# Performance work log

Hardware: AMD Instinct MI355X
Metric: run time of the kernel (lower is better)

## Reference

```python
import jax, jax.numpy as jnp
import numpy as np
from jax import lax

H = 64          # GRU hidden size
OUT_STEPS = 20  # output_seq_size


def _maxpool2(x):
    # x: [N, C, H, W] -> 2x2 max pool, stride 2, VALID
    return lax.reduce_window(x, -jnp.inf, lax.max, (1, 1, 2, 2), (1, 1, 2, 2), 'VALID')


def _conv(x, w, b):
    # NCHW / OIHW, VALID, stride 1
    y = lax.conv_general_dilated(x, w, (1, 1), 'VALID',
                                 dimension_numbers=('NCHW', 'OIHW', 'NCHW'))
    return y + b[None, :, None, None]


def _gru_step(h, x, wih, whh, bih, bhh):
    # PyTorch GRU gate order: r, z, n
    gi = x @ wih.T + bih            # [B, 3H]
    gh = h @ whh.T + bhh            # [B, 3H]
    i_r, i_z, i_n = jnp.split(gi, 3, axis=-1)
    h_r, h_z, h_n = jnp.split(gh, 3, axis=-1)
    r = jax.nn.sigmoid(i_r + h_r)
    z = jax.nn.sigmoid(i_z + h_z)
    n = jnp.tanh(i_n + r * h_n)
    return (1.0 - z) * n + z * h


def setup_inputs() -> dict:
    key = jax.random.key(0)
    ks = jax.random.split(key, 20)
    B, T = 1024, 31
    s = 0.1
    return {
        'bbox_seq': jax.random.normal(ks[0], (B, T, 4), jnp.float32),
        'head_seq': jax.random.uniform(ks[1], (B, T, 32, 32), jnp.float32),
        'conv1_w': jax.random.normal(ks[2], (4, 1, 3, 3), jnp.float32) * s,
        'conv1_b': jax.random.normal(ks[3], (4,), jnp.float32) * s,
        'conv2_w': jax.random.normal(ks[4], (10, 4, 3, 3), jnp.float32) * s,
        'conv2_b': jax.random.normal(ks[5], (10,), jnp.float32) * s,
        'fc_w': jax.random.normal(ks[6], (5, 360), jnp.float32) * s,
        'fc_b': jax.random.normal(ks[7], (5,), jnp.float32) * s,
        'enc_wih': jax.random.normal(ks[8], (3 * H, 9), jnp.float32) * s,
        'enc_whh': jax.random.normal(ks[9], (3 * H, H), jnp.float32) * s,
        'enc_bih': jax.random.normal(ks[10], (3 * H,), jnp.float32) * s,
        'enc_bhh': jax.random.normal(ks[11], (3 * H,), jnp.float32) * s,
        'dec_wih': jax.random.normal(ks[12], (3 * H, 4), jnp.float32) * s,
        'dec_whh': jax.random.normal(ks[13], (3 * H, H), jnp.float32) * s,
        'dec_bih': jax.random.normal(ks[14], (3 * H,), jnp.float32) * s,
        'dec_bhh': jax.random.normal(ks[15], (3 * H,), jnp.float32) * s,
        'lin_w': jax.random.normal(ks[16], (4, H), jnp.float32) * s,
        'lin_b': jax.random.normal(ks[17], (4,), jnp.float32) * s,
    }


def reference(bbox_seq, head_seq, conv1_w, conv1_b, conv2_w, conv2_b, fc_w, fc_b,
              enc_wih, enc_whh, enc_bih, enc_bhh,
              dec_wih, dec_whh, dec_bih, dec_bhh, lin_w, lin_b):
    B, T = bbox_seq.shape[0], bbox_seq.shape[1]
    L = T - 1  # encoder sequence length

    # offset: last bbox, broadcast over OUT_STEPS -> [B, OUT_STEPS, 4]
    offset = jnp.broadcast_to(bbox_seq[:, -1][:, None, :], (B, OUT_STEPS, 4))

    diffs = bbox_seq[:, 1:] - bbox_seq[:, :-1]  # [B, L, 4] (dropout p=0 -> identity)

    # --- ConvEncoder on all head crops at once ---
    imgs = head_seq[:, :-1].reshape(B * L, 1, 32, 32)
    x = jax.nn.relu(_conv(imgs, conv1_w, conv1_b))   # [BL, 4, 30, 30]
    x = _maxpool2(x)                                  # [BL, 4, 15, 15]
    x = jax.nn.relu(_conv(x, conv2_w, conv2_b))       # [BL, 10, 13, 13]
    x = _maxpool2(x)                                  # [BL, 10, 6, 6]
    emb = x.reshape(B * L, -1) @ fc_w.T + fc_b        # [BL, 5]
    emb = emb.reshape(B, L, -1)

    enc_in = jnp.concatenate([diffs, emb], axis=2)    # [B, L, 9]

    # --- GRU encoder (scan over time) ---
    def enc_step(h, x_t):
        h = _gru_step(h, x_t, enc_wih, enc_whh, enc_bih, enc_bhh)
        return h, None
    h0 = jnp.zeros((B, H), enc_in.dtype)
    hn, _ = lax.scan(enc_step, h0, jnp.swapaxes(enc_in, 0, 1))

    def dec_step(carry, _):
        h, prev_x = carry
        h = _gru_step(h, prev_x, dec_wih, dec_whh, dec_bih, dec_bhh)
        x_new = h @ lin_w.T + lin_b + prev_x
        return (h, x_new), x_new
    (_, _), outs = lax.scan(dec_step, (hn, diffs[:, -1]), None, length=OUT_STEPS)
    out = jnp.swapaxes(outs, 0, 1)                    # [B, OUT_STEPS, 4]

    return jnp.cumsum(out, axis=1) + offset
```

## Files before the change

kernel.cpp:

```cpp
#include <hip/hip_runtime.h>
#include <hip/hip_bf16.h>


#define B_    1024
#define L_    30
#define H_    64

typedef _Float16 half_t;
typedef __attribute__((ext_vector_type(8))) _Float16 half8;
typedef __attribute__((ext_vector_type(4))) float f32x4;

#define MFMA16(A, B, C) __builtin_amdgcn_mfma_f32_16x16x32_f16(A, B, C, 0, 0, 0)

__device__ __forceinline__ float sigmoid_f(float v) {
    return __builtin_amdgcn_rcpf(1.f + __expf(-v));
}
__device__ __forceinline__ float tanh_f(float v) {
    v = fminf(fmaxf(v, -15.f), 15.f);
    const float e = __expf(2.f * v);
    return (e - 1.f) * __builtin_amdgcn_rcpf(e + 1.f);
}
__device__ __forceinline__ void load4_lds(float* r, const float* p) {
    float2 a = *(const float2*)p;
    float2 b = *(const float2*)(p + 2);
    r[0] = a.x; r[1] = a.y; r[2] = b.x; r[3] = b.y;
}

__global__ __launch_bounds__(64) void conv_embed_kernel(
    const float* __restrict__ bbox,
    const float* __restrict__ head,
    const float* __restrict__ c1w, const float* __restrict__ c1b,
    const float* __restrict__ c2w, const float* __restrict__ c2b,
    const float* __restrict__ fcw, const float* __restrict__ fcb,
    float* __restrict__ enc_in)
{
    const int img = blockIdx.x;
    const int b = img / L_;
    const int l = img % L_;
    const int tid = threadIdx.x;

    __shared__ float s_img[32 * 32];
    __shared__ float s_p1[4 * 15 * 16];
    __shared__ float s_p2[360];
    __shared__ float s_red[60];

    {
        const float4* src = (const float4*)(head + ((size_t)b * 31 + (size_t)l) * 1024);
        float4* dst = (float4*)s_img;
        #pragma unroll
        for (int i = 0; i < 4; ++i) dst[tid + 64 * i] = src[tid + 64 * i];
    }
    __syncthreads();

    if (tid < 60) {
        const int c = tid / 15, px = tid % 15;
        const int x0 = 2 * px;
        float wg[9];
        #pragma unroll
        for (int k = 0; k < 9; ++k) wg[k] = c1w[c * 9 + k];
        const float bias = c1b[c];

        auto c1out = [&](const float* ra, const float* rb, const float* rc, const float* rd) -> float {
            float a00 = bias, a01 = bias, a10 = bias, a11 = bias;
            #pragma unroll
            for (int kx = 0; kx < 3; ++kx) {
                const float w0 = wg[kx], w1 = wg[3 + kx], w2 = wg[6 + kx];
                a00 = fmaf(w0, ra[kx],     fmaf(w1, rb[kx],     fmaf(w2, rc[kx],     a00)));
                a01 = fmaf(w0, ra[kx + 1], fmaf(w1, rb[kx + 1], fmaf(w2, rc[kx + 1], a01)));
                a10 = fmaf(w0, rb[kx],     fmaf(w1, rc[kx],     fmaf(w2, rd[kx],     a10)));
                a11 = fmaf(w0, rb[kx + 1], fmaf(w1, rc[kx + 1], fmaf(w2, rd[kx + 1], a11)));
            }
            a00 = fmaxf(a00, 0.f); a01 = fmaxf(a01, 0.f);
            a10 = fmaxf(a10, 0.f); a11 = fmaxf(a11, 0.f);
            return fmaxf(fmaxf(a00, a01), fmaxf(a10, a11));
        };

        float r[6][4];
        load4_lds(r[0], s_img + 0 * 32 + x0);
        load4_lds(r[1], s_img + 1 * 32 + x0);
        #pragma unroll
        for (int i = 0; i < 7; ++i) {
            const int s0 = (4 * i) % 6, s1 = (4 * i + 1) % 6, s2 = (4 * i + 2) % 6;
            const int s3 = (4 * i + 3) % 6, s4 = (4 * i + 4) % 6, s5 = (4 * i + 5) % 6;
            load4_lds(r[s2], s_img + (4 * i + 2) * 32 + x0);
            load4_lds(r[s3], s_img + (4 * i + 3) * 32 + x0);
            s_p1[c * 240 + (2 * i) * 16 + px] = c1out(r[s0], r[s1], r[s2], r[s3]);
            load4_lds(r[s4], s_img + (4 * i + 4) * 32 + x0);
            load4_lds(r[s5], s_img + (4 * i + 5) * 32 + x0);
            s_p1[c * 240 + (2 * i + 1) * 16 + px] = c1out(r[s2], r[s3], r[s4], r[s5]);
        }
        load4_lds(r[0], s_img + 30 * 32 + x0);
        load4_lds(r[1], s_img + 31 * 32 + x0);
        s_p1[c * 240 + 14 * 16 + px] = c1out(r[4], r[5], r[0], r[1]);
    }
    __syncthreads();

    if (tid < 60) {
        const int c = tid / 6, px = tid % 6;
        const int x0 = 2 * px;
        float wg2[4][9];
        #pragma unroll
        for (int ic = 0; ic < 4; ++ic)
            #pragma unroll
            for (int k = 0; k < 9; ++k) wg2[ic][k] = c2w[(c * 4 + ic) * 9 + k];
        const float bias2 = c2b[c];

        float P[6][4][4];
        auto c2out = [&](float (*pa)[4], float (*pb)[4], float (*pc)[4], float (*pd)[4]) -> float {
            float a00 = bias2, a01 = bias2, a10 = bias2, a11 = bias2;
            #pragma unroll
            for (int ic = 0; ic < 4; ++ic) {
                #pragma unroll
                for (int kx = 0; kx < 3; ++kx) {
                    const float w0 = wg2[ic][kx], w1 = wg2[ic][3 + kx], w2 = wg2[ic][6 + kx];
                    a00 = fmaf(w0, pa[ic][kx],     fmaf(w1, pb[ic][kx],     fmaf(w2, pc[ic][kx],     a00)));
                    a01 = fmaf(w0, pa[ic][kx + 1], fmaf(w1, pb[ic][kx + 1], fmaf(w2, pc[ic][kx + 1], a01)));
                    a10 = fmaf(w0, pb[ic][kx],     fmaf(w1, pc[ic][kx],     fmaf(w2, pd[ic][kx],     a10)));
                    a11 = fmaf(w0, pb[ic][kx + 1], fmaf(w1, pc[ic][kx + 1], fmaf(w2, pd[ic][kx + 1], a11)));
                }
            }
            a00 = fmaxf(a00, 0.f); a01 = fmaxf(a01, 0.f);
            a10 = fmaxf(a10, 0.f); a11 = fmaxf(a11, 0.f);
            return fmaxf(fmaxf(a00, a01), fmaxf(a10, a11));
        };

        #pragma unroll
        for (int ic = 0; ic < 4; ++ic) {
            load4_lds(P[0][ic], s_p1 + ic * 240 + 0 * 16 + x0);
            load4_lds(P[1][ic], s_p1 + ic * 240 + 1 * 16 + x0);
        }
        #pragma unroll
        for (int i = 0; i < 3; ++i) {
            const int s0 = (4 * i) % 6, s1 = (4 * i + 1) % 6, s2 = (4 * i + 2) % 6;
            const int s3 = (4 * i + 3) % 6, s4 = (4 * i + 4) % 6, s5 = (4 * i + 5) % 6;
            #pragma unroll
            for (int ic = 0; ic < 4; ++ic) {
                load4_lds(P[s2][ic], s_p1 + ic * 240 + (4 * i + 2) * 16 + x0);
                load4_lds(P[s3][ic], s_p1 + ic * 240 + (4 * i + 3) * 16 + x0);
            }
            s_p2[c * 36 + (2 * i) * 6 + px] = c2out(P[s0], P[s1], P[s2], P[s3]);
            #pragma unroll
            for (int ic = 0; ic < 4; ++ic) {
                load4_lds(P[s4][ic], s_p1 + ic * 240 + (4 * i + 4) * 16 + x0);
                load4_lds(P[s5][ic], s_p1 + ic * 240 + (4 * i + 5) * 16 + x0);
            }
            s_p2[c * 36 + (2 * i + 1) * 6 + px] = c2out(P[s2], P[s3], P[s4], P[s5]);
        }
    }
    __syncthreads();

    if (tid < 60) {
        const int o = tid / 12, i0 = tid % 12;
        const float* wrow = fcw + o * 360;
        float acc = 0.f;
        #pragma unroll
        for (int k = 0; k < 30; ++k) {
            const int i = i0 + 12 * k;
            acc = fmaf(wrow[i], s_p2[i], acc);
        }
        s_red[tid] = acc;
    }
    __syncthreads();

    float* dst = enc_in + ((size_t)b * L_ + l) * 9;
    if (tid < 5) {
        float acc = fcb[tid];
        #pragma unroll
        for (int k = 0; k < 12; ++k) acc += s_red[tid * 12 + k];
        dst[4 + tid] = acc;
    } else if (tid >= 8 && tid < 12) {
        const int d = tid - 8;
        const float* bb = bbox + (size_t)b * 124 + (size_t)l * 4;
        dst[d] = bb[4 + d] - bb[d];
    }
}

__global__ __launch_bounds__(256, 1) void gru_mfma_kernel(
    const float* __restrict__ bbox,
    const float* __restrict__ enc_in,
    const float* __restrict__ ewih, const float* __restrict__ ewhh,
    const float* __restrict__ ebih, const float* __restrict__ ebhh,
    const float* __restrict__ dwih, const float* __restrict__ dwhh,
    const float* __restrict__ dbih, const float* __restrict__ dbhh,
    const float* __restrict__ linw, const float* __restrict__ linb,
    float* __restrict__ out)
{
    const int bb  = blockIdx.x * 16;
    const int tid = threadIdx.x;
    const int w   = tid >> 6;
    const int l   = tid & 63;
    const int q   = l >> 4;
    const int col = l & 15;

    alignas(16) __shared__ half_t hbuf[2][16][72];
    alignas(16) __shared__ half_t xenc[30][16][40];
    alignas(16) __shared__ half_t xdec[16][40];

    {
        int4* p = (int4*)hbuf;
        for (int i = tid; i < (int)(sizeof(hbuf) / 16); i += 256) p[i] = int4{0, 0, 0, 0};
        p = (int4*)xenc;
        for (int i = tid; i < (int)(sizeof(xenc) / 16); i += 256) p[i] = int4{0, 0, 0, 0};
        p = (int4*)xdec;
        for (int i = tid; i < (int)(sizeof(xdec) / 16); i += 256) p[i] = int4{0, 0, 0, 0};
    }
    __syncthreads();

    for (int pr = tid; pr < 480; pr += 256) {
        const int t = pr / 16, b = pr % 16;
        const float* src = enc_in + ((size_t)(bb + b) * L_ + t) * 9;
        #pragma unroll
        for (int d = 0; d < 9; ++d) xenc[t][b][d] = (half_t)src[d];
    }

    float xold[4], ofs[4], cs[4];
    if (w == 0 && col < 4) {
        #pragma unroll
        for (int r = 0; r < 4; ++r) {
            const float* bbp = bbox + (size_t)(bb + q * 4 + r) * 124;
            xold[r] = bbp[120 + col] - bbp[116 + col];
            ofs[r]  = bbp[120 + col];
            cs[r]   = 0.f;
            xdec[q * 4 + r][col] = (half_t)xold[r];
        }
    }

    const int urow = 16 * w + col;
    auto whh_frag = [&](const float* W, int gate, int kap) -> half8 {
        const float* rp = W + (size_t)(gate * 64 + urow) * 64 + kap * 32 + q * 8;
        half8 f;
        #pragma unroll
        for (int j = 0; j < 8; ++j) f[j] = (half_t)rp[j];
        return f;
    };
    auto wih_frag = [&](const float* W, int gate, int indim) -> half8 {
        half8 f;
        #pragma unroll
        for (int j = 0; j < 8; ++j) {
            const int d = q * 8 + j;
            f[j] = (d < indim) ? (half_t)W[(size_t)(gate * 64 + urow) * indim + d]
                               : (half_t)0.f;
        }
        return f;
    };

    const half8 eBr0 = whh_frag(ewhh, 0, 0), eBr1 = whh_frag(ewhh, 0, 1);
    const half8 eBz0 = whh_frag(ewhh, 1, 0), eBz1 = whh_frag(ewhh, 1, 1);
    const half8 eBn0 = whh_frag(ewhh, 2, 0), eBn1 = whh_frag(ewhh, 2, 1);
    const half8 eBrx = wih_frag(ewih, 0, 9);
    const half8 eBzx = wih_frag(ewih, 1, 9);
    const half8 eBnx = wih_frag(ewih, 2, 9);

    const half8 dBr0 = whh_frag(dwhh, 0, 0), dBr1 = whh_frag(dwhh, 0, 1);
    const half8 dBz0 = whh_frag(dwhh, 1, 0), dBz1 = whh_frag(dwhh, 1, 1);
    const half8 dBn0 = whh_frag(dwhh, 2, 0), dBn1 = whh_frag(dwhh, 2, 1);
    const half8 dBrx = wih_frag(dwih, 0, 4);
    const half8 dBzx = wih_frag(dwih, 1, 4);
    const half8 dBnx = wih_frag(dwih, 2, 4);

    half8 Bl0, Bl1;
    #pragma unroll
    for (int j = 0; j < 8; ++j) {
        Bl0[j] = (col < 4) ? (half_t)linw[col * 64 +      q * 8 + j] : (half_t)0.f;
        Bl1[j] = (col < 4) ? (half_t)linw[col * 64 + 32 + q * 8 + j] : (half_t)0.f;
    }

    const float ebr  = ebih[urow]       + ebhh[urow];
    const float ebz  = ebih[64 + urow]  + ebhh[64 + urow];
    const float ebnh = ebhh[128 + urow];
    const float ebni = ebih[128 + urow];
    const float dbr  = dbih[urow]       + dbhh[urow];
    const float dbz  = dbih[64 + urow]  + dbhh[64 + urow];
    const float dbnh = dbhh[128 + urow];
    const float dbni = dbih[128 + urow];
    const float lb   = (col < 4) ? linb[col] : 0.f;

    float hold[4] = {0.f, 0.f, 0.f, 0.f};
    __syncthreads();

    for (int t = 0; t < L_; ++t) {
        const int p = t & 1;
        const half8 a0 = *(const half8*)&hbuf[p][col][q * 8];
        const half8 a1 = *(const half8*)&hbuf[p][col][32 + q * 8];
        const half8 a2 = *(const half8*)&xenc[t][col][q * 8];

        f32x4 Cr  = {ebr, ebr, ebr, ebr};
        f32x4 Cz  = {ebz, ebz, ebz, ebz};
        f32x4 Cnh = {ebnh, ebnh, ebnh, ebnh};
        f32x4 Cnx = {ebni, ebni, ebni, ebni};
        Cr  = MFMA16(a0, eBr0, Cr);  Cr  = MFMA16(a1, eBr1, Cr);  Cr = MFMA16(a2, eBrx, Cr);
        Cz  = MFMA16(a0, eBz0, Cz);  Cz  = MFMA16(a1, eBz1, Cz);  Cz = MFMA16(a2, eBzx, Cz);
        Cnh = MFMA16(a0, eBn0, Cnh); Cnh = MFMA16(a1, eBn1, Cnh);
        Cnx = MFMA16(a2, eBnx, Cnx);

        #pragma unroll
        for (int r = 0; r < 4; ++r) {
            const float rr = sigmoid_f(Cr[r]);
            const float zz = sigmoid_f(Cz[r]);
            const float nn = tanh_f(Cnx[r] + rr * Cnh[r]);
            hold[r] = fmaf(zz, hold[r] - nn, nn);
            hbuf[p ^ 1][q * 4 + r][urow] = (half_t)hold[r];
        }
        __syncthreads();
    }

    for (int tt = 0; tt < 20; ++tt) {
        const int p = tt & 1;
        const half8 a0 = *(const half8*)&hbuf[p][col][q * 8];
        const half8 a1 = *(const half8*)&hbuf[p][col][32 + q * 8];
        const half8 a2 = *(const half8*)&xdec[col][q * 8];

        f32x4 Cr  = {dbr, dbr, dbr, dbr};
        f32x4 Cz  = {dbz, dbz, dbz, dbz};
        f32x4 Cnh = {dbnh, dbnh, dbnh, dbnh};
        f32x4 Cnx = {dbni, dbni, dbni, dbni};
        Cr  = MFMA16(a0, dBr0, Cr);  Cr  = MFMA16(a1, dBr1, Cr);  Cr = MFMA16(a2, dBrx, Cr);
        Cz  = MFMA16(a0, dBz0, Cz);  Cz  = MFMA16(a1, dBz1, Cz);  Cz = MFMA16(a2, dBzx, Cz);
        Cnh = MFMA16(a0, dBn0, Cnh); Cnh = MFMA16(a1, dBn1, Cnh);
        Cnx = MFMA16(a2, dBnx, Cnx);

        #pragma unroll
        for (int r = 0; r < 4; ++r) {
            const float rr = sigmoid_f(Cr[r]);
            const float zz = sigmoid_f(Cz[r]);
            const float nn = tanh_f(Cnx[r] + rr * Cnh[r]);
            hold[r] = fmaf(zz, hold[r] - nn, nn);
            hbuf[p ^ 1][q * 4 + r][urow] = (half_t)hold[r];
        }
        __syncthreads();

        const half8 al0 = *(const half8*)&hbuf[p ^ 1][col][q * 8];
        const half8 al1 = *(const half8*)&hbuf[p ^ 1][col][32 + q * 8];
        f32x4 X = {0.f, 0.f, 0.f, 0.f};
        X = MFMA16(al0, Bl0, X);
        X = MFMA16(al1, Bl1, X);

        if (w == 0 && col < 4) {
            #pragma unroll
            for (int r = 0; r < 4; ++r) {
                const float xv = X[r] + lb + xold[r];
                xold[r] = xv;
                cs[r] += xv;
                xdec[q * 4 + r][col] = (half_t)xv;
                out[(size_t)(bb + q * 4 + r) * 80 + tt * 4 + col] = cs[r] + ofs[r];
            }
        }
        __syncthreads();
    }
}

extern "C" void kernel_launch(void* const* d_in, const int* in_sizes, int n_in,
                              void* d_out, int out_size, void* d_ws, size_t ws_size,
                              hipStream_t stream) {
    (void)in_sizes; (void)n_in; (void)out_size; (void)ws_size;
    const float* bbox = (const float*)d_in[0];
    const float* head = (const float*)d_in[1];
    const float* c1w  = (const float*)d_in[2];
    const float* c1b  = (const float*)d_in[3];
    const float* c2w  = (const float*)d_in[4];
    const float* c2b  = (const float*)d_in[5];
    const float* fcw  = (const float*)d_in[6];
    const float* fcb  = (const float*)d_in[7];
    const float* ewih = (const float*)d_in[8];
    const float* ewhh = (const float*)d_in[9];
    const float* ebih = (const float*)d_in[10];
    const float* ebhh = (const float*)d_in[11];
    const float* dwih = (const float*)d_in[12];
    const float* dwhh = (const float*)d_in[13];
    const float* dbih = (const float*)d_in[14];
    const float* dbhh = (const float*)d_in[15];
    const float* linw = (const float*)d_in[16];
    const float* linb = (const float*)d_in[17];
    float* out = (float*)d_out;

    float* enc_in = (float*)d_ws;

    conv_embed_kernel<<<B_ * L_, 64, 0, stream>>>(bbox, head, c1w, c1b, c2w, c2b,
                                                  fcw, fcb, enc_in);
    gru_mfma_kernel<<<B_ / 16, 256, 0, stream>>>(bbox, enc_in,
                                                 ewih, ewhh, ebih, ebhh,
                                                 dwih, dwhh, dbih, dbhh,
                                                 linw, linb, out);
}
```

Measured before the change: 284.0 us.

## Fuse conv embedding and GRU into one kernel with per-timestep counters

The two launches become one kernel. The first 64 blocks run the GRU, and the remaining blocks each process four images with their conv and embedding, ordered by timestep. After each timestep's images are stored, an atomic counter for that timestep is incremented. GRU blocks spin on that counter before loading their inputs, so the encoder recurrence overlaps with conv work for later timesteps. This relies on the GRU blocks being resident first and on co-scheduling, adds a memset and spin-waiting, and could deadlock if the GRU blocks are not scheduled.

Result: slower. 1.109 ms (+290.5%).

```diff
diff --git a/kernel.cpp b/kernel.cpp
--- a/kernel.cpp
+++ b/kernel.cpp
@@ -2,9 +2,10 @@
 #include <hip/hip_bf16.h>
 
 
-#define B_    1024
-#define L_    30
-#define H_    64
+#define B_      1024
+#define L_      30
+#define H_      64
+#define NGRUBLK 64
 
 typedef _Float16 half_t;
 typedef __attribute__((ext_vector_type(8))) _Float16 half8;
@@ -26,202 +27,194 @@
     r[0] = a.x; r[1] = a.y; r[2] = b.x; r[3] = b.y;
 }
 
-__global__ __launch_bounds__(64) void conv_embed_kernel(
+union alignas(16) SharedU {
+    struct {
+        half_t hbuf[2][16][72];
+        half_t xenc[16][40];
+        half_t xdec[16][40];
+    } g;
+    struct {
+        float s_img[32 * 32];
+        float s_p1[4 * 15 * 16];
+        float s_p2[360];
+        float s_red[60];
+    } c[4];
+};
+
+__global__ __launch_bounds__(256, 3) void fused_kernel(
     const float* __restrict__ bbox,
     const float* __restrict__ head,
     const float* __restrict__ c1w, const float* __restrict__ c1b,
     const float* __restrict__ c2w, const float* __restrict__ c2b,
     const float* __restrict__ fcw, const float* __restrict__ fcb,
-    float* __restrict__ enc_in)
-{
-    const int img = blockIdx.x;
-    const int b = img / L_;
-    const int l = img % L_;
-    const int tid = threadIdx.x;
-
-    __shared__ float s_img[32 * 32];
-    __shared__ float s_p1[4 * 15 * 16];
-    __shared__ float s_p2[360];
-    __shared__ float s_red[60];
-
-    {
-        const float4* src = (const float4*)(head + ((size_t)b * 31 + (size_t)l) * 1024);
-        float4* dst = (float4*)s_img;
-        #pragma unroll
-        for (int i = 0; i < 4; ++i) dst[tid + 64 * i] = src[tid + 64 * i];
-    }
-    __syncthreads();
-
-    if (tid < 60) {
-        const int c = tid / 15, px = tid % 15;
-        const int x0 = 2 * px;
-        float wg[9];
-        #pragma unroll
-        for (int k = 0; k < 9; ++k) wg[k] = c1w[c * 9 + k];
-        const float bias = c1b[c];
-
-        auto c1out = [&](const float* ra, const float* rb, const float* rc, const float* rd) -> float {
-            float a00 = bias, a01 = bias, a10 = bias, a11 = bias;
-            #pragma unroll
-            for (int kx = 0; kx < 3; ++kx) {
-                const float w0 = wg[kx], w1 = wg[3 + kx], w2 = wg[6 + kx];
-                a00 = fmaf(w0, ra[kx],     fmaf(w1, rb[kx],     fmaf(w2, rc[kx],     a00)));
-                a01 = fmaf(w0, ra[kx + 1], fmaf(w1, rb[kx + 1], fmaf(w2, rc[kx + 1], a01)));
-                a10 = fmaf(w0, rb[kx],     fmaf(w1, rc[kx],     fmaf(w2, rd[kx],     a10)));
-                a11 = fmaf(w0, rb[kx + 1], fmaf(w1, rc[kx + 1], fmaf(w2, rd[kx + 1], a11)));
-            }
-            a00 = fmaxf(a00, 0.f); a01 = fmaxf(a01, 0.f);
-            a10 = fmaxf(a10, 0.f); a11 = fmaxf(a11, 0.f);
-            return fmaxf(fmaxf(a00, a01), fmaxf(a10, a11));
-        };
-
-        float r[6][4];
-        load4_lds(r[0], s_img + 0 * 32 + x0);
-        load4_lds(r[1], s_img + 1 * 32 + x0);
-        #pragma unroll
-        for (int i = 0; i < 7; ++i) {
-            const int s0 = (4 * i) % 6, s1 = (4 * i + 1) % 6, s2 = (4 * i + 2) % 6;
-            const int s3 = (4 * i + 3) % 6, s4 = (4 * i + 4) % 6, s5 = (4 * i + 5) % 6;
-            load4_lds(r[s2], s_img + (4 * i + 2) * 32 + x0);
-            load4_lds(r[s3], s_img + (4 * i + 3) * 32 + x0);
-            s_p1[c * 240 + (2 * i) * 16 + px] = c1out(r[s0], r[s1], r[s2], r[s3]);
-            load4_lds(r[s4], s_img + (4 * i + 4) * 32 + x0);
-            load4_lds(r[s5], s_img + (4 * i + 5) * 32 + x0);
-            s_p1[c * 240 + (2 * i + 1) * 16 + px] = c1out(r[s2], r[s3], r[s4], r[s5]);
-        }
-        load4_lds(r[0], s_img + 30 * 32 + x0);
-        load4_lds(r[1], s_img + 31 * 32 + x0);
-        s_p1[c * 240 + 14 * 16 + px] = c1out(r[4], r[5], r[0], r[1]);
-    }
-    __syncthreads();
-
-    if (tid < 60) {
-        const int c = tid / 6, px = tid % 6;
-        const int x0 = 2 * px;
-        float wg2[4][9];
-        #pragma unroll
-        for (int ic = 0; ic < 4; ++ic)
-            #pragma unroll
-            for (int k = 0; k < 9; ++k) wg2[ic][k] = c2w[(c * 4 + ic) * 9 + k];
-        const float bias2 = c2b[c];
-
-        float P[6][4][4];
-        auto c2out = [&](float (*pa)[4], float (*pb)[4], float (*pc)[4], float (*pd)[4]) -> float {
-            float a00 = bias2, a01 = bias2, a10 = bias2, a11 = bias2;
-            #pragma unroll
-            for (int ic = 0; ic < 4; ++ic) {
-                #pragma unroll
-                for (int kx = 0; kx < 3; ++kx) {
-                    const float w0 = wg2[ic][kx], w1 = wg2[ic][3 + kx], w2 = wg2[ic][6 + kx];
-                    a00 = fmaf(w0, pa[ic][kx],     fmaf(w1, pb[ic][kx],     fmaf(w2, pc[ic][kx],     a00)));
-                    a01 = fmaf(w0, pa[ic][kx + 1], fmaf(w1, pb[ic][kx + 1], fmaf(w2, pc[ic][kx + 1], a01)));
-                    a10 = fmaf(w0, pb[ic][kx],     fmaf(w1, pc[ic][kx],     fmaf(w2, pd[ic][kx],     a10)));
-                    a11 = fmaf(w0, pb[ic][kx + 1], fmaf(w1, pc[ic][kx + 1], fmaf(w2, pd[ic][kx + 1], a11)));
-                }
-            }
-            a00 = fmaxf(a00, 0.f); a01 = fmaxf(a01, 0.f);
-            a10 = fmaxf(a10, 0.f); a11 = fmaxf(a11, 0.f);
-            return fmaxf(fmaxf(a00, a01), fmaxf(a10, a11));
-        };
-
-        #pragma unroll
-        for (int ic = 0; ic < 4; ++ic) {
-            load4_lds(P[0][ic], s_p1 + ic * 240 + 0 * 16 + x0);
-            load4_lds(P[1][ic], s_p1 + ic * 240 + 1 * 16 + x0);
-        }
-        #pragma unroll
-        for (int i = 0; i < 3; ++i) {
-            const int s0 = (4 * i) % 6, s1 = (4 * i + 1) % 6, s2 = (4 * i + 2) % 6;
-            const int s3 = (4 * i + 3) % 6, s4 = (4 * i + 4) % 6, s5 = (4 * i + 5) % 6;
-            #pragma unroll
-            for (int ic = 0; ic < 4; ++ic) {
-                load4_lds(P[s2][ic], s_p1 + ic * 240 + (4 * i + 2) * 16 + x0);
-                load4_lds(P[s3][ic], s_p1 + ic * 240 + (4 * i + 3) * 16 + x0);
-            }
-            s_p2[c * 36 + (2 * i) * 6 + px] = c2out(P[s0], P[s1], P[s2], P[s3]);
-            #pragma unroll
-            for (int ic = 0; ic < 4; ++ic) {
-                load4_lds(P[s4][ic], s_p1 + ic * 240 + (4 * i + 4) * 16 + x0);
-                load4_lds(P[s5][ic], s_p1 + ic * 240 + (4 * i + 5) * 16 + x0);
-            }
-            s_p2[c * 36 + (2 * i + 1) * 6 + px] = c2out(P[s2], P[s3], P[s4], P[s5]);
-        }
-    }
-    __syncthreads();
-
-    if (tid < 60) {
-        const int o = tid / 12, i0 = tid % 12;
-        const float* wrow = fcw + o * 360;
-        float acc = 0.f;
-        #pragma unroll
-        for (int k = 0; k < 30; ++k) {
-            const int i = i0 + 12 * k;
-            acc = fmaf(wrow[i], s_p2[i], acc);
-        }
-        s_red[tid] = acc;
-    }
-    __syncthreads();
-
-    float* dst = enc_in + ((size_t)b * L_ + l) * 9;
-    if (tid < 5) {
-        float acc = fcb[tid];
-        #pragma unroll
-        for (int k = 0; k < 12; ++k) acc += s_red[tid * 12 + k];
-        dst[4 + tid] = acc;
-    } else if (tid >= 8 && tid < 12) {
-        const int d = tid - 8;
-        const float* bb = bbox + (size_t)b * 124 + (size_t)l * 4;
-        dst[d] = bb[4 + d] - bb[d];
-    }
-}
-
-__global__ __launch_bounds__(256, 1) void gru_mfma_kernel(
-    const float* __restrict__ bbox,
-    const float* __restrict__ enc_in,
     const float* __restrict__ ewih, const float* __restrict__ ewhh,
     const float* __restrict__ ebih, const float* __restrict__ ebhh,
     const float* __restrict__ dwih, const float* __restrict__ dwhh,
     const float* __restrict__ dbih, const float* __restrict__ dbhh,
     const float* __restrict__ linw, const float* __restrict__ linb,
+    float* __restrict__ enc_in,
+    unsigned*            ctr,
     float* __restrict__ out)
 {
-    const int bb  = blockIdx.x * 16;
+    __shared__ SharedU su;
     const int tid = threadIdx.x;
+
+    if (blockIdx.x >= NGRUBLK) {
+        const int sub  = tid >> 6;
+        const int lane = tid & 63;
+        const int img  = (((int)blockIdx.x - NGRUBLK) << 2) | sub;
+        const int ts   = img >> 10;
+        const int b    = img & 1023;
+        auto& S = su.c[sub];
+
+        {
+            const float4* src = (const float4*)(head + ((size_t)b * 31 + (size_t)ts) * 1024);
+            float4* dstv = (float4*)S.s_img;
+            #pragma unroll
+            for (int i = 0; i < 4; ++i) dstv[lane + 64 * i] = src[lane + 64 * i];
+        }
+        __syncthreads();
+
+        if (lane < 60) {
+            const int c = lane / 15, px = lane % 15;
+            const int x0 = 2 * px;
+            float wg[9];
+            #pragma unroll
+            for (int k = 0; k < 9; ++k) wg[k] = c1w[c * 9 + k];
+            const float bias = c1b[c];
+
+            auto c1out = [&](const float* ra, const float* rb, const float* rc, const float* rd) -> float {
+                float a00 = bias, a01 = bias, a10 = bias, a11 = bias;
+                #pragma unroll
+                for (int kx = 0; kx < 3; ++kx) {
+                    const float w0 = wg[kx], w1 = wg[3 + kx], w2 = wg[6 + kx];
+                    a00 = fmaf(w0, ra[kx],     fmaf(w1, rb[kx],     fmaf(w2, rc[kx],     a00)));
+                    a01 = fmaf(w0, ra[kx + 1], fmaf(w1, rb[kx + 1], fmaf(w2, rc[kx + 1], a01)));
+                    a10 = fmaf(w0, rb[kx],     fmaf(w1, rc[kx],     fmaf(w2, rd[kx],     a10)));
+                    a11 = fmaf(w0, rb[kx + 1], fmaf(w1, rc[kx + 1], fmaf(w2, rd[kx + 1], a11)));
+                }
+                a00 = fmaxf(a00, 0.f); a01 = fmaxf(a01, 0.f);
+                a10 = fmaxf(a10, 0.f); a11 = fmaxf(a11, 0.f);
+                return fmaxf(fmaxf(a00, a01), fmaxf(a10, a11));
+            };
+
+            float r[6][4];
+            load4_lds(r[0], S.s_img + 0 * 32 + x0);
+            load4_lds(r[1], S.s_img + 1 * 32 + x0);
+            #pragma unroll
+            for (int i = 0; i < 7; ++i) {
+                const int s0 = (4 * i) % 6, s1 = (4 * i + 1) % 6, s2 = (4 * i + 2) % 6;
+                const int s3 = (4 * i + 3) % 6, s4 = (4 * i + 4) % 6, s5 = (4 * i + 5) % 6;
+                load4_lds(r[s2], S.s_img + (4 * i + 2) * 32 + x0);
+                load4_lds(r[s3], S.s_img + (4 * i + 3) * 32 + x0);
+                S.s_p1[c * 240 + (2 * i) * 16 + px] = c1out(r[s0], r[s1], r[s2], r[s3]);
+                load4_lds(r[s4], S.s_img + (4 * i + 4) * 32 + x0);
+                load4_lds(r[s5], S.s_img + (4 * i + 5) * 32 + x0);
+                S.s_p1[c * 240 + (2 * i + 1) * 16 + px] = c1out(r[s2], r[s3], r[s4], r[s5]);
+            }
+            load4_lds(r[0], S.s_img + 30 * 32 + x0);
+            load4_lds(r[1], S.s_img + 31 * 32 + x0);
+            S.s_p1[c * 240 + 14 * 16 + px] = c1out(r[4], r[5], r[0], r[1]);
+        }
+        __syncthreads();
+
+        if (lane < 60) {
+            const int c = lane / 6, px = lane % 6;
+            const int x0 = 2 * px;
+            float wg2[4][9];
+            #pragma unroll
+            for (int ic = 0; ic < 4; ++ic)
+                #pragma unroll
+                for (int k = 0; k < 9; ++k) wg2[ic][k] = c2w[(c * 4 + ic) * 9 + k];
+            const float bias2 = c2b[c];
+
+            float P[6][4][4];
+            auto c2out = [&](float (*pa)[4], float (*pb)[4], float (*pc)[4], float (*pd)[4]) -> float {
+                float a00 = bias2, a01 = bias2, a10 = bias2, a11 = bias2;
+                #pragma unroll
+                for (int ic = 0; ic < 4; ++ic) {
+                    #pragma unroll
+                    for (int kx = 0; kx < 3; ++kx) {
+                        const float w0 = wg2[ic][kx], w1 = wg2[ic][3 + kx], w2 = wg2[ic][6 + kx];
+                        a00 = fmaf(w0, pa[ic][kx],     fmaf(w1, pb[ic][kx],     fmaf(w2, pc[ic][kx],     a00)));
+                        a01 = fmaf(w0, pa[ic][kx + 1], fmaf(w1, pb[ic][kx + 1], fmaf(w2, pc[ic][kx + 1], a01)));
+                        a10 = fmaf(w0, pb[ic][kx],     fmaf(w1, pc[ic][kx],     fmaf(w2, pd[ic][kx],     a10)));
+                        a11 = fmaf(w0, pb[ic][kx + 1], fmaf(w1, pc[ic][kx + 1], fmaf(w2, pd[ic][kx + 1], a11)));
+                    }
+                }
+                a00 = fmaxf(a00, 0.f); a01 = fmaxf(a01, 0.f);
+                a10 = fmaxf(a10, 0.f); a11 = fmaxf(a11, 0.f);
+                return fmaxf(fmaxf(a00, a01), fmaxf(a10, a11));
+            };
+
+            #pragma unroll
+            for (int ic = 0; ic < 4; ++ic) {
+                load4_lds(P[0][ic], S.s_p1 + ic * 240 + 0 * 16 + x0);
+                load4_lds(P[1][ic], S.s_p1 + ic * 240 + 1 * 16 + x0);
+            }
+            #pragma unroll
+            for (int i = 0; i < 3; ++i) {
+                const int s0 = (4 * i) % 6, s1 = (4 * i + 1) % 6, s2 = (4 * i + 2) % 6;
+                const int s3 = (4 * i + 3) % 6, s4 = (4 * i + 4) % 6, s5 = (4 * i + 5) % 6;
+                #pragma unroll
+                for (int ic = 0; ic < 4; ++ic) {
+                    load4_lds(P[s2][ic], S.s_p1 + ic * 240 + (4 * i + 2) * 16 + x0);
+                    load4_lds(P[s3][ic], S.s_p1 + ic * 240 + (4 * i + 3) * 16 + x0);
+                }
+                S.s_p2[c * 36 + (2 * i) * 6 + px] = c2out(P[s0], P[s1], P[s2], P[s3]);
+                #pragma unroll
+                for (int ic = 0; ic < 4; ++ic) {
+                    load4_lds(P[s4][ic], S.s_p1 + ic * 240 + (4 * i + 4) * 16 + x0);
+                    load4_lds(P[s5][ic], S.s_p1 + ic * 240 + (4 * i + 5) * 16 + x0);
+                }
+                S.s_p2[c * 36 + (2 * i + 1) * 6 + px] = c2out(P[s2], P[s3], P[s4], P[s5]);
+            }
+        }
+        __syncthreads();
+
+        if (lane < 60) {
+            const int o = lane / 12, i0 = lane % 12;
+            const float* wrow = fcw + o * 360;
+            float acc = 0.f;
+            #pragma unroll
+            for (int k = 0; k < 30; ++k) {
+                const int i = i0 + 12 * k;
+                acc = fmaf(wrow[i], S.s_p2[i], acc);
+            }
+            S.s_red[lane] = acc;
+        }
+        __syncthreads();
+
+        float* dst = enc_in + ((size_t)b * L_ + ts) * 9;
+        if (lane < 5) {
+            float acc = fcb[lane];
+            #pragma unroll
+            for (int k = 0; k < 12; ++k) acc += S.s_red[lane * 12 + k];
+            __hip_atomic_store(&dst[4 + lane], acc, __ATOMIC_RELAXED, __HIP_MEMORY_SCOPE_AGENT);
+        } else if (lane >= 8 && lane < 12) {
+            const int d = lane - 8;
+            const float* bbp = bbox + (size_t)b * 124 + (size_t)ts * 4;
+            __hip_atomic_store(&dst[d], bbp[4 + d] - bbp[d], __ATOMIC_RELAXED, __HIP_MEMORY_SCOPE_AGENT);
+        }
+        __syncthreads();
+        if (lane == 0)
+            __hip_atomic_fetch_add(&ctr[ts], 1u, __ATOMIC_RELEASE, __HIP_MEMORY_SCOPE_AGENT);
+        return;
+    }
+
+    const int bb  = (int)blockIdx.x * 16;
     const int w   = tid >> 6;
     const int l   = tid & 63;
     const int q   = l >> 4;
     const int col = l & 15;
-
-    alignas(16) __shared__ half_t hbuf[2][16][72];
-    alignas(16) __shared__ half_t xenc[30][16][40];
-    alignas(16) __shared__ half_t xdec[16][40];
+    auto& G = su.g;
 
     {
-        int4* p = (int4*)hbuf;
-        for (int i = tid; i < (int)(sizeof(hbuf) / 16); i += 256) p[i] = int4{0, 0, 0, 0};
-        p = (int4*)xenc;
-        for (int i = tid; i < (int)(sizeof(xenc) / 16); i += 256) p[i] = int4{0, 0, 0, 0};
-        p = (int4*)xdec;
-        for (int i = tid; i < (int)(sizeof(xdec) / 16); i += 256) p[i] = int4{0, 0, 0, 0};
-    }
-    __syncthreads();
-
-    for (int pr = tid; pr < 480; pr += 256) {
-        const int t = pr / 16, b = pr % 16;
-        const float* src = enc_in + ((size_t)(bb + b) * L_ + t) * 9;
-        #pragma unroll
-        for (int d = 0; d < 9; ++d) xenc[t][b][d] = (half_t)src[d];
-    }
-
-    float xold[4], ofs[4], cs[4];
-    if (w == 0 && col < 4) {
-        #pragma unroll
-        for (int r = 0; r < 4; ++r) {
-            const float* bbp = bbox + (size_t)(bb + q * 4 + r) * 124;
-            xold[r] = bbp[120 + col] - bbp[116 + col];
-            ofs[r]  = bbp[120 + col];
-            cs[r]   = 0.f;
-            xdec[q * 4 + r][col] = (half_t)xold[r];
+        int4* p = (int4*)&G;
+        #pragma unroll
+        for (int i = 0; i < 2; ++i) {
+            const int idx = tid + 256 * i;
+            if (idx < (int)(sizeof(G) / 16)) p[idx] = int4{0, 0, 0, 0};
         }
     }
 
@@ -251,38 +244,34 @@
     const half8 eBzx = wih_frag(ewih, 1, 9);
     const half8 eBnx = wih_frag(ewih, 2, 9);
 
-    const half8 dBr0 = whh_frag(dwhh, 0, 0), dBr1 = whh_frag(dwhh, 0, 1);
-    const half8 dBz0 = whh_frag(dwhh, 1, 0), dBz1 = whh_frag(dwhh, 1, 1);
-    const half8 dBn0 = whh_frag(dwhh, 2, 0), dBn1 = whh_frag(dwhh, 2, 1);
-    const half8 dBrx = wih_frag(dwih, 0, 4);
-    const half8 dBzx = wih_frag(dwih, 1, 4);
-    const half8 dBnx = wih_frag(dwih, 2, 4);
-
-    half8 Bl0, Bl1;
-    #pragma unroll
-    for (int j = 0; j < 8; ++j) {
-        Bl0[j] = (col < 4) ? (half_t)linw[col * 64 +      q * 8 + j] : (half_t)0.f;
-        Bl1[j] = (col < 4) ? (half_t)linw[col * 64 + 32 + q * 8 + j] : (half_t)0.f;
-    }
-
     const float ebr  = ebih[urow]       + ebhh[urow];
     const float ebz  = ebih[64 + urow]  + ebhh[64 + urow];
     const float ebnh = ebhh[128 + urow];
     const float ebni = ebih[128 + urow];
-    const float dbr  = dbih[urow]       + dbhh[urow];
-    const float dbz  = dbih[64 + urow]  + dbhh[64 + urow];
-    const float dbnh = dbhh[128 + urow];
-    const float dbni = dbih[128 + urow];
-    const float lb   = (col < 4) ? linb[col] : 0.f;
 
     float hold[4] = {0.f, 0.f, 0.f, 0.f};
     __syncthreads();
 
     for (int t = 0; t < L_; ++t) {
+        if (tid == 0) {
+            while (__hip_atomic_load(&ctr[t], __ATOMIC_ACQUIRE, __HIP_MEMORY_SCOPE_AGENT)
+                   < (unsigned)B_)
+                __builtin_amdgcn_s_sleep(2);
+        }
+        __syncthreads();
+        if (tid < 144) {
+            const int bq = tid / 9, d = tid - 9 * bq;
+            const float v = __hip_atomic_load(
+                &enc_in[((size_t)(bb + bq) * L_ + t) * 9 + d],
+                __ATOMIC_RELAXED, __HIP_MEMORY_SCOPE_AGENT);
+            G.xenc[bq][d] = (half_t)v;
+        }
+        __syncthreads();
+
         const int p = t & 1;
-        const half8 a0 = *(const half8*)&hbuf[p][col][q * 8];
-        const half8 a1 = *(const half8*)&hbuf[p][col][32 + q * 8];
-        const half8 a2 = *(const half8*)&xenc[t][col][q * 8];
+        const half8 a0 = *(const half8*)&G.hbuf[p][col][q * 8];
+        const half8 a1 = *(const half8*)&G.hbuf[p][col][32 + q * 8];
+        const half8 a2 = *(const half8*)&G.xenc[col][q * 8];
 
         f32x4 Cr  = {ebr, ebr, ebr, ebr};
         f32x4 Cz  = {ebz, ebz, ebz, ebz};
@@ -299,16 +288,49 @@
             const float zz = sigmoid_f(Cz[r]);
             const float nn = tanh_f(Cnx[r] + rr * Cnh[r]);
             hold[r] = fmaf(zz, hold[r] - nn, nn);
-            hbuf[p ^ 1][q * 4 + r][urow] = (half_t)hold[r];
-        }
-        __syncthreads();
-    }
+            G.hbuf[p ^ 1][q * 4 + r][urow] = (half_t)hold[r];
+        }
+        __syncthreads();
+    }
+
+    const half8 dBr0 = whh_frag(dwhh, 0, 0), dBr1 = whh_frag(dwhh, 0, 1);
+    const half8 dBz0 = whh_frag(dwhh, 1, 0), dBz1 = whh_frag(dwhh, 1, 1);
+    const half8 dBn0 = whh_frag(dwhh, 2, 0), dBn1 = whh_frag(dwhh, 2, 1);
+    const half8 dBrx = wih_frag(dwih, 0, 4);
+    const half8 dBzx = wih_frag(dwih, 1, 4);
+    const half8 dBnx = wih_frag(dwih, 2, 4);
+
+    half8 Bl0, Bl1;
+    #pragma unroll
+    for (int j = 0; j < 8; ++j) {
+        Bl0[j] = (col < 4) ? (half_t)linw[col * 64 +      q * 8 + j] : (half_t)0.f;
+        Bl1[j] = (col < 4) ? (half_t)linw[col * 64 + 32 + q * 8 + j] : (half_t)0.f;
+    }
+
+    const float dbr  = dbih[urow]       + dbhh[urow];
+    const float dbz  = dbih[64 + urow]  + dbhh[64 + urow];
+    const float dbnh = dbhh[128 + urow];
+    const float dbni = dbih[128 + urow];
+    const float lb   = (col < 4) ? linb[col] : 0.f;
+
+    float xold[4], ofs[4], cs[4];
+    if (w == 0 && col < 4) {
+        #pragma unroll
+        for (int r = 0; r < 4; ++r) {
+            const float* bbp = bbox + (size_t)(bb + q * 4 + r) * 124;
+            xold[r] = bbp[120 + col] - bbp[116 + col];
+            ofs[r]  = bbp[120 + col];
+            cs[r]   = 0.f;
+            G.xdec[q * 4 + r][col] = (half_t)xold[r];
+        }
+    }
+    __syncthreads();
 
     for (int tt = 0; tt < 20; ++tt) {
         const int p = tt & 1;
-        const half8 a0 = *(const half8*)&hbuf[p][col][q * 8];
-        const half8 a1 = *(const half8*)&hbuf[p][col][32 + q * 8];
-        const half8 a2 = *(const half8*)&xdec[col][q * 8];
+        const half8 a0 = *(const half8*)&G.hbuf[p][col][q * 8];
+        const half8 a1 = *(const half8*)&G.hbuf[p][col][32 + q * 8];
+        const half8 a2 = *(const half8*)&G.xdec[col][q * 8];
 
         f32x4 Cr  = {dbr, dbr, dbr, dbr};
         f32x4 Cz  = {dbz, dbz, dbz, dbz};
@@ -325,12 +347,12 @@
             const float zz = sigmoid_f(Cz[r]);
             const float nn = tanh_f(Cnx[r] + rr * Cnh[r]);
             hold[r] = fmaf(zz, hold[r] - nn, nn);
-            hbuf[p ^ 1][q * 4 + r][urow] = (half_t)hold[r];
-        }
-        __syncthreads();
-
-        const half8 al0 = *(const half8*)&hbuf[p ^ 1][col][q * 8];
-        const half8 al1 = *(const half8*)&hbuf[p ^ 1][col][32 + q * 8];
+            G.hbuf[p ^ 1][q * 4 + r][urow] = (half_t)hold[r];
+        }
+        __syncthreads();
+
+        const half8 al0 = *(const half8*)&G.hbuf[p ^ 1][col][q * 8];
+        const half8 al1 = *(const half8*)&G.hbuf[p ^ 1][col][32 + q * 8];
         f32x4 X = {0.f, 0.f, 0.f, 0.f};
         X = MFMA16(al0, Bl0, X);
         X = MFMA16(al1, Bl1, X);
@@ -341,7 +363,7 @@
                 const float xv = X[r] + lb + xold[r];
                 xold[r] = xv;
                 cs[r] += xv;
-                xdec[q * 4 + r][col] = (half_t)xv;
+                G.xdec[q * 4 + r][col] = (half_t)xv;
                 out[(size_t)(bb + q * 4 + r) * 80 + tt * 4 + col] = cs[r] + ofs[r];
             }
         }
@@ -373,12 +395,14 @@
     const float* linb = (const float*)d_in[17];
     float* out = (float*)d_out;
 
-    float* enc_in = (float*)d_ws;
-
-    conv_embed_kernel<<<B_ * L_, 64, 0, stream>>>(bbox, head, c1w, c1b, c2w, c2b,
-                                                  fcw, fcb, enc_in);
-    gru_mfma_kernel<<<B_ / 16, 256, 0, stream>>>(bbox, enc_in,
-                                                 ewih, ewhh, ebih, ebhh,
-                                                 dwih, dwhh, dbih, dbhh,
-                                                 linw, linb, out);
+    float*    enc_in = (float*)d_ws;
+    unsigned* ctr    = (unsigned*)((char*)d_ws + (size_t)B_ * L_ * 9 * sizeof(float));
+
+    hipMemsetAsync(ctr, 0, 32 * sizeof(unsigned), stream);
+
+    const int grid = NGRUBLK + (B_ * L_) / 4;
+    fused_kernel<<<grid, 256, 0, stream>>>(bbox, head, c1w, c1b, c2w, c2b,
+                                           fcw, fcb, ewih, ewhh, ebih, ebhh,
+                                           dwih, dwhh, dbih, dbhh, linw, linb,
+                                           enc_in, ctr, out);
 }
```
